# Kernel optimization log

Measured on AMD Instinct MI355X. Metric: run time of the kernel, lower is better.

Reference implementation:

```python
import jax, jax.numpy as jnp
import numpy as np
from math import sqrt

B, L, S = 4, 2048, 2048
D_MODEL, H = 1024, 16
E = D_MODEL // H  # head dim = 64


def setup_inputs() -> dict:
    key = jax.random.key(0)
    ks = jax.random.split(key, 11)
    s = 1.0 / sqrt(D_MODEL)
    return {
        "queries": jax.random.normal(ks[0], (B, L, D_MODEL), jnp.float32),
        "keys": jax.random.normal(ks[1], (B, S, D_MODEL), jnp.float32),
        "values": jax.random.normal(ks[2], (B, S, D_MODEL), jnp.float32),
        "Wq": jax.random.normal(ks[3], (D_MODEL, D_MODEL), jnp.float32) * s,
        "bq": jax.random.normal(ks[4], (D_MODEL,), jnp.float32) * s,
        "Wk": jax.random.normal(ks[5], (D_MODEL, D_MODEL), jnp.float32) * s,
        "bk": jax.random.normal(ks[6], (D_MODEL,), jnp.float32) * s,
        "Wv": jax.random.normal(ks[7], (D_MODEL, D_MODEL), jnp.float32) * s,
        "bv": jax.random.normal(ks[8], (D_MODEL,), jnp.float32) * s,
        "Wo": jax.random.normal(ks[9], (D_MODEL, D_MODEL), jnp.float32) * s,
        "bo": jax.random.normal(ks[10], (D_MODEL,), jnp.float32) * s,
    }


def reference(queries, keys, values, Wq, bq, Wk, bk, Wv, bv, Wo, bo):
    # QKV projections, split heads: [B, L/S, H, E]
    q = (queries @ Wq + bq).reshape(B, L, H, E)
    k = (keys @ Wk + bk).reshape(B, S, H, E)
    v = (values @ Wv + bv).reshape(B, S, H, E)
    scale = 1.0 / sqrt(E)
    scores = jnp.einsum('blhe,bshe->bhls', q, k)  # [B,H,L,S]
    A = jax.nn.softmax(scale * scores, axis=-1)   # dropout is identity in eval
    out = jnp.einsum('bhls,bshd->blhd', A, v).reshape(B, L, H * E)
    return out @ Wo + bo
```

## Files before the change

kernel.cpp:

```cpp
#include <hip/hip_runtime.h>
#include <hip/hip_bf16.h>

typedef unsigned short u16;
typedef unsigned int u32;
using short8 = __attribute__((ext_vector_type(8))) short;
using f32x4  = __attribute__((ext_vector_type(4))) float;
using f32x16 = __attribute__((ext_vector_type(16))) float;
using u32x2  = __attribute__((ext_vector_type(2))) unsigned int;
using u32x4  = __attribute__((ext_vector_type(4))) unsigned int;

#define B_  4
#define L_  2048
#define S_  2048
#define DM  1024
#define H_  16
#define E_  64

__device__ __forceinline__ u16 f2bf(float f) {
  union { float f; unsigned u; } v; v.f = f;
  unsigned u = v.u;
  unsigned r = (u + 0x7fffu + ((u >> 16) & 1u)) >> 16;
  return (u16)r;
}

__device__ __forceinline__ float exp2a(float x) {
  float r; asm("v_exp_f32 %0, %1" : "=v"(r) : "v"(x)); return r;
}

__device__ __forceinline__ u32 cvtpk(float lo, float hi) {
  u32 r; asm("v_cvt_pk_bf16_f32 %0, %1, %2" : "=v"(r) : "v"(lo), "v"(hi));
  return r;
}

__device__ __forceinline__ f32x4 mfma16(short8 a, short8 b, f32x4 c) {
  return __builtin_amdgcn_mfma_f32_16x16x32_bf16(a, b, c, 0, 0, 0);
}

__device__ __forceinline__ f32x16 mfma32(short8 a, short8 b, f32x16 c) {
  return __builtin_amdgcn_mfma_f32_32x32x16_bf16(a, b, c, 0, 0, 0);
}

__device__ __forceinline__ void gload_lds16(const u16* g, u16* l) {
  __builtin_amdgcn_global_load_lds(
      (const __attribute__((address_space(1))) unsigned int*)(const void*)g,
      (__attribute__((address_space(3))) unsigned int*)(void*)l, 16, 0, 0);
}

__global__ __launch_bounds__(256) void transp_all(const float* __restrict__ w0,
                                                  const float* __restrict__ w1,
                                                  const float* __restrict__ w2,
                                                  const float* __restrict__ w3,
                                                  u16* __restrict__ t0,
                                                  u16* __restrict__ t1,
                                                  u16* __restrict__ t2,
                                                  u16* __restrict__ t3) {
  const float* W = blockIdx.z == 0 ? w0 : blockIdx.z == 1 ? w1 :
                   blockIdx.z == 2 ? w2 : w3;
  u16* Wt = blockIdx.z == 0 ? t0 : blockIdx.z == 1 ? t1 :
            blockIdx.z == 2 ? t2 : t3;
  __shared__ float t[32][33];
  int tx = threadIdx.x & 31, ty = (threadIdx.x >> 5) & 7;
#pragma unroll
  for (int j = 0; j < 32; j += 8)
    t[ty + j][tx] = W[(size_t)(blockIdx.y * 32 + ty + j) * DM + blockIdx.x * 32 + tx];
  __syncthreads();
#pragma unroll
  for (int j = 0; j < 32; j += 8)
    Wt[(size_t)(blockIdx.x * 32 + ty + j) * DM + blockIdx.y * 32 + tx] = f2bf(t[tx][ty + j]);
}

template <int EPI>
__device__ __forceinline__ void gemm_body(const float* __restrict__ A,
                                          const u16* __restrict__ Bt,
                                          const float* __restrict__ bias,
                                          void* __restrict__ Cout,
                                          int M, int N, int K, float oscale,
                                          int bx, int by) {
  __shared__ u16 lA[128 * 32];
  __shared__ u16 lB[128 * 32];
  const int tid = threadIdx.x, wid = tid >> 6, lane = tid & 63;
  const int lr = lane & 15, lh = lane >> 4;
  const int m0 = by * 128, n0 = bx * 128;
  const int wr = wid >> 1, wc = wid & 1;

  f32x4 acc[4][4];
#pragma unroll
  for (int m = 0; m < 4; m++)
#pragma unroll
    for (int n = 0; n < 4; n++) acc[m][n] = (f32x4){0.f, 0.f, 0.f, 0.f};

  const int srow = wid * 16 + (lane >> 2);
  const int scol = (lane & 3) * 8;

  const float* a0p = A + (size_t)(m0 + srow) * K + scol;
  const float* a1p = A + (size_t)(m0 + 64 + srow) * K + scol;

  f32x4 r00 = *(const f32x4*)a0p;
  f32x4 r01 = *(const f32x4*)(a0p + 4);
  f32x4 r10 = *(const f32x4*)a1p;
  f32x4 r11 = *(const f32x4*)(a1p + 4);

  for (int k0 = 0; k0 < K; k0 += 32) {
    gload_lds16(Bt + (size_t)(n0 + srow) * K + k0 + scol, lB + (wid * 16) * 32);
    gload_lds16(Bt + (size_t)(n0 + 64 + srow) * K + k0 + scol, lB + (64 + wid * 16) * 32);
    u32x4 w0 = {cvtpk(r00.x, r00.y), cvtpk(r00.z, r00.w),
                cvtpk(r01.x, r01.y), cvtpk(r01.z, r01.w)};
    u32x4 w1 = {cvtpk(r10.x, r10.y), cvtpk(r10.z, r10.w),
                cvtpk(r11.x, r11.y), cvtpk(r11.z, r11.w)};
    *(u32x4*)(lA + (size_t)srow * 32 + scol) = w0;
    *(u32x4*)(lA + (size_t)(64 + srow) * 32 + scol) = w1;
    if (k0 + 32 < K) {
      r00 = *(const f32x4*)(a0p + k0 + 32);
      r01 = *(const f32x4*)(a0p + k0 + 36);
      r10 = *(const f32x4*)(a1p + k0 + 32);
      r11 = *(const f32x4*)(a1p + k0 + 36);
    }
    __syncthreads();
    short8 af[4], bf[4];
#pragma unroll
    for (int m = 0; m < 4; m++)
      af[m] = *(const short8*)(lA + (wr * 64 + m * 16 + lr) * 32 + lh * 8);
#pragma unroll
    for (int n = 0; n < 4; n++)
      bf[n] = *(const short8*)(lB + (wc * 64 + n * 16 + lr) * 32 + lh * 8);
#pragma unroll
    for (int m = 0; m < 4; m++)
#pragma unroll
      for (int n = 0; n < 4; n++) acc[m][n] = mfma16(af[m], bf[n], acc[m][n]);
    __syncthreads();
  }

#pragma unroll
  for (int m = 0; m < 4; m++) {
    int grow0 = m0 + wr * 64 + m * 16 + lh * 4;
#pragma unroll
    for (int n = 0; n < 4; n++) {
      int gcol = n0 + wc * 64 + n * 16 + lr;
      float bi = bias[gcol];
      float v0 = (acc[m][n][0] + bi) * oscale;
      float v1 = (acc[m][n][1] + bi) * oscale;
      float v2 = (acc[m][n][2] + bi) * oscale;
      float v3 = (acc[m][n][3] + bi) * oscale;
      u32 p01 = cvtpk(v0, v1), p23 = cvtpk(v2, v3);
      u16* C = (u16*)Cout;
#pragma unroll
      for (int r = 0; r < 4; r++) {
        u32 pk = r < 2 ? p01 : p23;
        u16 bv = (r & 1) ? (u16)(pk >> 16) : (u16)(pk & 0xffff);
        int grow = grow0 + r;
        if constexpr (EPI == 0) {
          C[(size_t)grow * N + gcol] = bv;
        } else {
          int bb = grow >> 11, sl = grow & 2047;
          C[((size_t)(bb * DM) + gcol) * S_ + sl] = bv;
        }
      }
    }
  }
}

__global__ __launch_bounds__(256) void gemm_qkv(
    const float* __restrict__ q, const float* __restrict__ k, const float* __restrict__ v,
    const u16* __restrict__ WqT, const u16* __restrict__ WkT, const u16* __restrict__ WvT,
    const float* __restrict__ bq, const float* __restrict__ bk, const float* __restrict__ bv,
    u16* __restrict__ Qp, u16* __restrict__ Kp, u16* __restrict__ Vt, float qsc) {
  int lin = blockIdx.x;
  int swz = (lin & 7) * 192 + (lin >> 3);
  const int bx = swz & 7, by = (swz >> 3) & 63, z = swz >> 9;
  if (z == 0)
    gemm_body<0>(q, WqT, bq, Qp, B_ * L_, DM, DM, qsc, bx, by);
  else if (z == 1)
    gemm_body<0>(k, WkT, bk, Kp, B_ * L_, DM, DM, 1.0f, bx, by);
  else
    gemm_body<1>(v, WvT, bv, Vt, B_ * L_, DM, DM, 1.0f, bx, by);
}

__global__ __launch_bounds__(256) void gemm_out(const u16* __restrict__ A,
                                                const u16* __restrict__ Bt,
                                                const float* __restrict__ bias,
                                                float* __restrict__ C) {
  const int N = DM, K = DM;
  int lin = blockIdx.x;
  int swz = (lin & 7) * 64 + (lin >> 3);
  const int bx = swz & 7, by = swz >> 3;

  __shared__ u16 lA[128 * 64];
  __shared__ u16 lB[128 * 64];
  const int tid = threadIdx.x, wid = tid >> 6, lane = tid & 63;
  const int lr = lane & 15, lh = lane >> 4;
  const int m0 = by * 128, n0 = bx * 128;
  const int wr = wid >> 1, wc = wid & 1;

  f32x4 acc[4][4];
#pragma unroll
  for (int m = 0; m < 4; m++)
#pragma unroll
    for (int n = 0; n < 4; n++) acc[m][n] = (f32x4){0.f, 0.f, 0.f, 0.f};

  const int sr = lane >> 3;
  const int scx = ((lane & 7) ^ (sr & 7)) * 8;
  const int sxr = (lr & 7) * 8;

  for (int k0 = 0; k0 < K; k0 += 64) {
#pragma unroll
    for (int p = 0; p < 4; p++) {
      int row = wid * 32 + p * 8 + sr;
      gload_lds16(A + (size_t)(m0 + row) * K + k0 + scx, lA + (wid * 32 + p * 8) * 64);
      gload_lds16(Bt + (size_t)(n0 + row) * K + k0 + scx, lB + (wid * 32 + p * 8) * 64);
    }
    __syncthreads();
#pragma unroll
    for (int s = 0; s < 2; s++) {
      short8 af[4], bf[4];
#pragma unroll
      for (int m = 0; m < 4; m++)
        af[m] = *(const short8*)(lA + (wr * 64 + m * 16 + lr) * 64 + ((s * 32 + lh * 8) ^ sxr));
#pragma unroll
      for (int n = 0; n < 4; n++)
        bf[n] = *(const short8*)(lB + (wc * 64 + n * 16 + lr) * 64 + ((s * 32 + lh * 8) ^ sxr));
#pragma unroll
      for (int m = 0; m < 4; m++)
#pragma unroll
        for (int n = 0; n < 4; n++) acc[m][n] = mfma16(af[m], bf[n], acc[m][n]);
    }
    __syncthreads();
  }

#pragma unroll
  for (int m = 0; m < 4; m++) {
    int grow0 = m0 + wr * 64 + m * 16 + lh * 4;
#pragma unroll
    for (int n = 0; n < 4; n++) {
      int gcol = n0 + wc * 64 + n * 16 + lr;
      float bi = bias[gcol];
#pragma unroll
      for (int r = 0; r < 4; r++)
        C[(size_t)(grow0 + r) * N + gcol] = acc[m][n][r] + bi;
    }
  }
}

__global__ __launch_bounds__(512) void attn(const u16* __restrict__ Q,
                                            const u16* __restrict__ Kp,
                                            const u16* __restrict__ Vt,
                                            u16* __restrict__ O) {
  __shared__ u16 lK[2][64 * 64];
  __shared__ u16 lV[2][64 * 64];
  const int tid = threadIdx.x, wid = tid >> 6, lane = tid & 63;
  const int l31 = lane & 31, hi = lane >> 5;

  int lin = blockIdx.x;
  int swz = (lin & 7) * 64 + (lin >> 3);
  const int bh = swz >> 3, q0 = (swz & 7) * 256;
  const int b = bh >> 4, h = bh & 15;
  const int qrow = q0 + wid * 32 + l31;

  const u16* Qb = Q + ((size_t)(b * L_ + qrow)) * DM + h * E_ + hi * 8;
  short8 qf[4];
#pragma unroll
  for (int s = 0; s < 4; s++) qf[s] = *(const short8*)(Qb + s * 16);

  f32x16 o[2];
#pragma unroll
  for (int et = 0; et < 2; et++)
#pragma unroll
    for (int r = 0; r < 16; r++) o[et][r] = 0.f;
  float m_r = -3.0e38f, l_r = 0.f;

  const u16* Kb = Kp + ((size_t)(b * S_)) * DM + h * E_;
  const u16* Vb = Vt + ((size_t)(b * DM + h * E_)) * S_;

  const int srow = wid * 8 + (lane >> 3);
  const u16* srcK = Kb + (size_t)srow * DM + ((lane & 7) ^ (srow & 7)) * 8;
  const u16* srcV = Vb + (size_t)srow * S_ + ((lane & 7) ^ (srow & 7)) * 8;

  const int sxk = (l31 & 7) * 8;
  const int hi4 = hi * 4, hi8 = hi * 8;

  auto stage = [&](int buf, int kb) {
    gload_lds16(srcK + (size_t)kb * DM, lK[buf] + wid * 512);
    gload_lds16(srcV + kb, lV[buf] + wid * 512);
  };

  stage(0, 0);
  const int NT = S_ / 64;
  for (int it = 0; it < NT; ++it) {
    const int buf = it & 1;
    __syncthreads();
    if (it + 1 < NT) stage(buf ^ 1, (it + 1) * 64);

    f32x16 sc[2];
    const u16* kbase = lK[buf] + l31 * 64;
    __builtin_amdgcn_s_setprio(1);
#pragma unroll
    for (int kt = 0; kt < 2; kt++) {
      f32x16 a;
#pragma unroll
      for (int r = 0; r < 16; r++) a[r] = 0.f;
#pragma unroll
      for (int s = 0; s < 4; s++) {
        short8 kf = *(const short8*)(kbase + kt * 2048 + ((s * 16 + hi8) ^ sxk));
        a = mfma32(kf, qf[s], a);
      }
      sc[kt] = a;
    }
    __builtin_amdgcn_s_setprio(0);

    f32x16 mA;
#pragma unroll
    for (int r = 0; r < 16; r++) mA[r] = fmaxf(sc[0][r], sc[1][r]);
#pragma unroll
    for (int r = 0; r < 8; r++) mA[r] = fmaxf(mA[r], mA[r + 8]);
#pragma unroll
    for (int r = 0; r < 4; r++) mA[r] = fmaxf(mA[r], mA[r + 4]);
    float tm = fmaxf(fmaxf(mA[0], mA[1]), fmaxf(mA[2], mA[3]));
    tm = fmaxf(tm, __shfl_xor(tm, 32));

    if (__any(tm > m_r + 8.f)) {
      float mn = fmaxf(m_r, tm);
      float al = exp2a(m_r - mn);
      m_r = mn;
      l_r *= al;
#pragma unroll
      for (int et = 0; et < 2; et++)
#pragma unroll
        for (int r = 0; r < 16; r++) o[et][r] *= al;
    }

    u32 wp[2][8];
    float rs = 0.f;
#pragma unroll
    for (int kt = 0; kt < 2; kt++)
#pragma unroll
      for (int i = 0; i < 8; i++) {
        float p0 = exp2a(sc[kt][2 * i] - m_r);
        float p1 = exp2a(sc[kt][2 * i + 1] - m_r);
        rs += p0 + p1;
        wp[kt][i] = cvtpk(p0, p1);
      }
    rs += __shfl_xor(rs, 32);
    l_r += rs;

    __builtin_amdgcn_s_setprio(1);
#pragma unroll
    for (int et = 0; et < 2; et++) {
      const u16* vp = lV[buf] + (et * 32 + l31) * 64;
#pragma unroll
      for (int kt = 0; kt < 2; kt++)
#pragma unroll
        for (int su = 0; su < 2; su++) {
          int koff = kt * 32 + su * 16 + hi4;
          u32x2 lo = *(const u32x2*)(vp + (koff ^ sxk));
          u32x2 hp = *(const u32x2*)(vp + ((koff + 8) ^ sxk));
          u32x4 vv = {lo.x, lo.y, hp.x, hp.y};
          u32x4 pv = {wp[kt][su * 4 + 0], wp[kt][su * 4 + 1],
                      wp[kt][su * 4 + 2], wp[kt][su * 4 + 3]};
          o[et] = mfma32(*(const short8*)&vv, *(const short8*)&pv, o[et]);
        }
    }
    __builtin_amdgcn_s_setprio(0);
  }

  float inv = 1.f / l_r;
  u16* Ob = O + ((size_t)(b * L_ + qrow)) * DM + h * E_;
#pragma unroll
  for (int et = 0; et < 2; et++)
#pragma unroll
    for (int t = 0; t < 4; t++) {
      u32x2 pk;
      pk.x = cvtpk(o[et][4 * t] * inv, o[et][4 * t + 1] * inv);
      pk.y = cvtpk(o[et][4 * t + 2] * inv, o[et][4 * t + 3] * inv);
      *(u32x2*)(Ob + et * 32 + t * 8 + hi4) = pk;
    }
}

extern "C" void kernel_launch(void* const* d_in, const int* in_sizes, int n_in,
                              void* d_out, int out_size, void* d_ws, size_t ws_size,
                              hipStream_t stream) {
  (void)in_sizes; (void)n_in; (void)out_size; (void)ws_size;
  const float* q  = (const float*)d_in[0];
  const float* k  = (const float*)d_in[1];
  const float* v  = (const float*)d_in[2];
  const float* Wq = (const float*)d_in[3];
  const float* bq = (const float*)d_in[4];
  const float* Wk = (const float*)d_in[5];
  const float* bk = (const float*)d_in[6];
  const float* Wv = (const float*)d_in[7];
  const float* bv = (const float*)d_in[8];
  const float* Wo = (const float*)d_in[9];
  const float* bo = (const float*)d_in[10];

  char* w = (char*)d_ws;
  const size_t ACT = (size_t)B_ * L_ * DM * 2;
  const size_t WT  = (size_t)DM * DM * 2;
  u16* WqT = (u16*)w; w += WT;
  u16* WkT = (u16*)w; w += WT;
  u16* WvT = (u16*)w; w += WT;
  u16* WoT = (u16*)w; w += WT;
  u16* Qp  = (u16*)w; w += ACT;
  u16* Kp  = (u16*)w; w += ACT;
  u16* Vt  = (u16*)w; w += ACT;
  u16* At  = (u16*)w; w += ACT;

  transp_all<<<dim3(32, 32, 4), 256, 0, stream>>>(Wq, Wk, Wv, Wo, WqT, WkT, WvT, WoT);

  const float QSC = 0.125f * 1.44269504089f;
  gemm_qkv<<<dim3(1536), 256, 0, stream>>>(
      q, k, v, WqT, WkT, WvT, bq, bk, bv, Qp, Kp, Vt, QSC);

  attn<<<dim3(512), 512, 0, stream>>>(Qp, Kp, Vt, At);

  gemm_out<<<dim3(512), 256, 0, stream>>>(At, WoT, bo, (float*)d_out);
}
```

Before: 208.4 us.

## Split attention KV sequence across two warp groups and merge in LDS

Doubles the attention block to 1024 threads, with two 8-wave groups each processing half of the key/value sequence (16 tiles each) using their own LDS buffers. The partial softmax states (max, sum, output accumulators) of group 1 are passed through LDS and merged into group 0 with exp2 rescaling before the final store. The aim is more waves in flight per CU to hide latency on the 512-block grid. In exchange it adds merge synchronisation and LDS traffic, and the per-wave register budget under launch_bounds(1024) may be tight.

```diff
diff --git a/kernel.cpp b/kernel.cpp
--- a/kernel.cpp
+++ b/kernel.cpp
@@ -240,20 +240,22 @@
   }
 }
 
-__global__ __launch_bounds__(512) void attn(const u16* __restrict__ Q,
-                                            const u16* __restrict__ Kp,
-                                            const u16* __restrict__ Vt,
-                                            u16* __restrict__ O) {
-  __shared__ u16 lK[2][64 * 64];
-  __shared__ u16 lV[2][64 * 64];
+__global__ __launch_bounds__(1024, 8) void attn(const u16* __restrict__ Q,
+                                                const u16* __restrict__ Kp,
+                                                const u16* __restrict__ Vt,
+                                                u16* __restrict__ O) {
+  __shared__ u16 smem[32768];
   const int tid = threadIdx.x, wid = tid >> 6, lane = tid & 63;
   const int l31 = lane & 31, hi = lane >> 5;
+  const int grp = wid >> 3, gw = wid & 7;
 
   int lin = blockIdx.x;
   int swz = (lin & 7) * 64 + (lin >> 3);
   const int bh = swz >> 3, q0 = (swz & 7) * 256;
   const int b = bh >> 4, h = bh & 15;
-  const int qrow = q0 + wid * 32 + l31;
+  const int qrow = q0 + gw * 32 + l31;
+
+  u16* gbase = smem + grp * 16384;
 
   const u16* Qb = Q + ((size_t)(b * L_ + qrow)) * DM + h * E_ + hi * 8;
   short8 qf[4];
@@ -270,27 +272,27 @@
   const u16* Kb = Kp + ((size_t)(b * S_)) * DM + h * E_;
   const u16* Vb = Vt + ((size_t)(b * DM + h * E_)) * S_;
 
-  const int srow = wid * 8 + (lane >> 3);
-  const u16* srcK = Kb + (size_t)srow * DM + ((lane & 7) ^ (srow & 7)) * 8;
-  const u16* srcV = Vb + (size_t)srow * S_ + ((lane & 7) ^ (srow & 7)) * 8;
+  const int srow = gw * 8 + (lane >> 3);
+  const u16* srcK = Kb + (size_t)(grp * 1024 + srow) * DM + ((lane & 7) ^ (srow & 7)) * 8;
+  const u16* srcV = Vb + (size_t)srow * S_ + grp * 1024 + ((lane & 7) ^ (srow & 7)) * 8;
 
   const int sxk = (l31 & 7) * 8;
   const int hi4 = hi * 4, hi8 = hi * 8;
 
-  auto stage = [&](int buf, int kb) {
-    gload_lds16(srcK + (size_t)kb * DM, lK[buf] + wid * 512);
-    gload_lds16(srcV + kb, lV[buf] + wid * 512);
+  auto stage = [&](int buf, int t) {
+    gload_lds16(srcK + (size_t)(t * 64) * DM, gbase + buf * 4096 + gw * 512);
+    gload_lds16(srcV + t * 64, gbase + 8192 + buf * 4096 + gw * 512);
   };
 
   stage(0, 0);
-  const int NT = S_ / 64;
+  const int NT = 16;
   for (int it = 0; it < NT; ++it) {
     const int buf = it & 1;
     __syncthreads();
-    if (it + 1 < NT) stage(buf ^ 1, (it + 1) * 64);
+    if (it + 1 < NT) stage(buf ^ 1, it + 1);
 
     f32x16 sc[2];
-    const u16* kbase = lK[buf] + l31 * 64;
+    const u16* kbase = gbase + buf * 4096 + l31 * 64;
     __builtin_amdgcn_s_setprio(1);
 #pragma unroll
     for (int kt = 0; kt < 2; kt++) {
@@ -344,7 +346,7 @@
     __builtin_amdgcn_s_setprio(1);
 #pragma unroll
     for (int et = 0; et < 2; et++) {
-      const u16* vp = lV[buf] + (et * 32 + l31) * 64;
+      const u16* vp = gbase + 8192 + buf * 4096 + (et * 32 + l31) * 64;
 #pragma unroll
       for (int kt = 0; kt < 2; kt++)
 #pragma unroll
@@ -361,17 +363,61 @@
     __builtin_amdgcn_s_setprio(0);
   }
 
-  float inv = 1.f / l_r;
-  u16* Ob = O + ((size_t)(b * L_ + qrow)) * DM + h * E_;
-#pragma unroll
-  for (int et = 0; et < 2; et++)
-#pragma unroll
-    for (int t = 0; t < 4; t++) {
-      u32x2 pk;
-      pk.x = cvtpk(o[et][4 * t] * inv, o[et][4 * t + 1] * inv);
-      pk.y = cvtpk(o[et][4 * t + 2] * inv, o[et][4 * t + 3] * inv);
-      *(u32x2*)(Ob + et * 32 + t * 8 + hi4) = pk;
-    }
+  float* cb = (float*)smem;
+  const int slot = gw * 64 + lane;
+  __syncthreads();
+  if (grp == 1) {
+    cb[8192 + slot] = m_r;
+    cb[8704 + slot] = l_r;
+#pragma unroll
+    for (int j = 0; j < 4; j++) {
+      f32x4 t = {o[0][4 * j], o[0][4 * j + 1], o[0][4 * j + 2], o[0][4 * j + 3]};
+      *(f32x4*)(cb + j * 2048 + slot * 4) = t;
+    }
+  }
+  __syncthreads();
+  float f0 = 0.f, f1 = 0.f;
+  if (grp == 0) {
+    float m1 = cb[8192 + slot], l1 = cb[8704 + slot];
+    float mn = fmaxf(m_r, m1);
+    f0 = exp2a(m_r - mn);
+    f1 = exp2a(m1 - mn);
+    l_r = l_r * f0 + l1 * f1;
+#pragma unroll
+    for (int j = 0; j < 4; j++) {
+      f32x4 t = *(const f32x4*)(cb + j * 2048 + slot * 4);
+#pragma unroll
+      for (int r = 0; r < 4; r++) o[0][4 * j + r] = o[0][4 * j + r] * f0 + t[r] * f1;
+    }
+  }
+  __syncthreads();
+  if (grp == 1) {
+#pragma unroll
+    for (int j = 0; j < 4; j++) {
+      f32x4 t = {o[1][4 * j], o[1][4 * j + 1], o[1][4 * j + 2], o[1][4 * j + 3]};
+      *(f32x4*)(cb + j * 2048 + slot * 4) = t;
+    }
+  }
+  __syncthreads();
+  if (grp == 0) {
+#pragma unroll
+    for (int j = 0; j < 4; j++) {
+      f32x4 t = *(const f32x4*)(cb + j * 2048 + slot * 4);
+#pragma unroll
+      for (int r = 0; r < 4; r++) o[1][4 * j + r] = o[1][4 * j + r] * f0 + t[r] * f1;
+    }
+    float inv = 1.f / l_r;
+    u16* Ob = O + ((size_t)(b * L_ + qrow)) * DM + h * E_;
+#pragma unroll
+    for (int et = 0; et < 2; et++)
+#pragma unroll
+      for (int t = 0; t < 4; t++) {
+        u32x2 pk;
+        pk.x = cvtpk(o[et][4 * t] * inv, o[et][4 * t + 1] * inv);
+        pk.y = cvtpk(o[et][4 * t + 2] * inv, o[et][4 * t + 3] * inv);
+        *(u32x2*)(Ob + et * 32 + t * 8 + hi4) = pk;
+      }
+  }
 }
 
 extern "C" void kernel_launch(void* const* d_in, const int* in_sizes, int n_in,
@@ -408,7 +454,7 @@
   gemm_qkv<<<dim3(1536), 256, 0, stream>>>(
       q, k, v, WqT, WkT, WvT, bq, bk, bv, Qp, Kp, Vt, QSC);
 
-  attn<<<dim3(512), 512, 0, stream>>>(Qp, Kp, Vt, At);
+  attn<<<dim3(512), 1024, 0, stream>>>(Qp, Kp, Vt, At);
 
   gemm_out<<<dim3(512), 256, 0, stream>>>(At, WoT, bo, (float*)d_out);
 }
```

Measured after the change: 698.6 us. 235% more time.
